# Kernel tuning notes

Measured on AMD Instinct MI355X. Metric: run time of the kernel, lower is better.

Reference implementation:

```python
import jax, jax.numpy as jnp
import numpy as np

NUM_PTS = 1024
LATENT_SIZE = 32
BETA = 0.1


def setup_inputs() -> dict:
    key = jax.random.key(0)
    k1, k2, k3, k4 = jax.random.split(key, 4)
    B = 128
    return {
        "recon_x": jax.random.normal(k1, (B, NUM_PTS, 3), dtype=jnp.float32),
        "x": jax.random.normal(k2, (B, NUM_PTS, 3), dtype=jnp.float32),
        "mu": jax.random.normal(k3, (B, LATENT_SIZE), dtype=jnp.float32),
        "logvar": jax.random.normal(k4, (B, LATENT_SIZE), dtype=jnp.float32),
    }


def _chamfer(recon_x, x):
    # Batched squared pairwise distances: P[b, i, j] = ||x[b,i] - recon_x[b,j]||^2
    xx = jnp.sum(x * x, axis=-1)              # [B, N]
    yy = jnp.sum(recon_x * recon_x, axis=-1)  # [B, N]
    xy = jnp.einsum("bnd,bmd->bnm", x, recon_x)  # [B, N, N]
    P = xx[:, :, None] + yy[:, None, :] - 2.0 * xy
    # Bidirectional min + sum
    loss_1 = jnp.sum(jnp.min(P, axis=1))  # for each recon point, nearest x point
    loss_2 = jnp.sum(jnp.min(P, axis=2))  # for each x point, nearest recon point
    return loss_1 + loss_2


def reference(recon_x, x, mu, logvar):
    RE = _chamfer(recon_x, x) / NUM_PTS
    KLD = -0.5 * jnp.sum(1.0 + logvar - mu * mu - jnp.exp(logvar))
    KLD = KLD / LATENT_SIZE
    return RE + KLD * BETA
```

## Files before the change

kernel.cpp:

```cpp
#include <hip/hip_runtime.h>

#define NUM_PTS 1024
#define NBATCH 128
#define BTHREADS 128
#define THREADS 256
#define NCHUNK 8
#define CHUNK_PTS (NUM_PTS / NCHUNK)
#define CHAMF_SCALE (1.0f / 1024.0f)
#define KLD_SCALE   (-0.5f * 0.1f / 32.0f)

#define WS_CHUNK_STRIDE (NBATCH * NUM_PTS)
#define WS_DIR_STRIDE   (NCHUNK * WS_CHUNK_STRIDE)

__global__ __launch_bounds__(BTHREADS, 4) void chamfer_part(
    const float* __restrict__ recon_x,
    const float* __restrict__ x,
    float* __restrict__ ws)
{
    const int b     = blockIdx.x >> 4;
    const int sub   = blockIdx.x & 15;
    const int dir   = sub >> 3;
    const int chunk = sub & 7;

    const float* rp = (dir == 0 ? x : recon_x) + (size_t)b * NUM_PTS * 3;
    const float* qp = (dir == 0 ? recon_x : x) + (size_t)b * NUM_PTS * 3
                      + chunk * CHUNK_PTS * 3;

    __shared__ float sq[4][CHUNK_PTS];
    {
        const int p = threadIdx.x;
        const float qx = qp[3 * p + 0];
        const float qy = qp[3 * p + 1];
        const float qz = qp[3 * p + 2];
        sq[0][p] = qx;
        sq[1][p] = qy;
        sq[2][p] = qz;
        sq[3][p] = fmaf(qx, qx, fmaf(qy, qy, qz * qz));
    }

    float buf[24];
    {
        const float4* __restrict__ src = (const float4*)(rp + 24 * threadIdx.x);
        float4* bp = (float4*)buf;
#pragma unroll
        for (int i = 0; i < 6; ++i) bp[i] = src[i];
    }
    float vx[8], vy[8], vz[8], r2[8], m[8];
#pragma unroll
    for (int k = 0; k < 8; ++k) {
        const float px = buf[3 * k + 0];
        const float py = buf[3 * k + 1];
        const float pz = buf[3 * k + 2];
        r2[k] = fmaf(px, px, fmaf(py, py, pz * pz));
        vx[k] = -2.0f * px;
        vy[k] = -2.0f * py;
        vz[k] = -2.0f * pz;
        m[k]  = 1e30f;
    }
    __syncthreads();

    const float4* __restrict__ sx4 = (const float4*)sq[0];
    const float4* __restrict__ sy4 = (const float4*)sq[1];
    const float4* __restrict__ sz4 = (const float4*)sq[2];
    const float4* __restrict__ s24 = (const float4*)sq[3];
#pragma unroll 2
    for (int t = 0; t < CHUNK_PTS / 4; ++t) {
        const float4 qx = sx4[t];
        const float4 qy = sy4[t];
        const float4 qz = sz4[t];
        const float4 q2 = s24[t];
#pragma unroll
        for (int jp = 0; jp < 2; ++jp) {
            const int j0 = 2 * jp, j1 = 2 * jp + 1;
            const float ax0 = (&qx.x)[j0], ay0 = (&qy.x)[j0],
                        az0 = (&qz.x)[j0], aq0 = (&q2.x)[j0];
            const float ax1 = (&qx.x)[j1], ay1 = (&qy.x)[j1],
                        az1 = (&qz.x)[j1], aq1 = (&q2.x)[j1];
            float d0[8], d1[8];
#pragma unroll
            for (int r = 0; r < 8; ++r)
                d0[r] = fmaf(vx[r], ax0, fmaf(vy[r], ay0, fmaf(vz[r], az0, aq0)));
#pragma unroll
            for (int r = 0; r < 8; ++r)
                d1[r] = fmaf(vx[r], ax1, fmaf(vy[r], ay1, fmaf(vz[r], az1, aq1)));
#pragma unroll
            for (int r = 0; r < 8; ++r)
                m[r] = fminf(fminf(m[r], d0[r]), d1[r]);
        }
    }

    float4* dst = (float4*)(ws + dir * WS_DIR_STRIDE + chunk * WS_CHUNK_STRIDE
                            + b * NUM_PTS + 8 * threadIdx.x);
    dst[0] = make_float4(r2[0] + m[0], r2[1] + m[1], r2[2] + m[2], r2[3] + m[3]);
    dst[1] = make_float4(r2[4] + m[4], r2[5] + m[5], r2[6] + m[6], r2[7] + m[7]);
}

__global__ __launch_bounds__(THREADS) void reduce_kernel(
    const float* __restrict__ ws,
    const float* __restrict__ mu,
    const float* __restrict__ logvar,
    float* __restrict__ out)
{
    const int gid  = blockIdx.x * THREADS + threadIdx.x;
    const int base = gid * 4;
    const int dir  = base >> 17;
    const int rem  = base & 131071;

    const float4* p = (const float4*)(ws + dir * WS_DIR_STRIDE + rem);
    float4 mn = p[0];
#pragma unroll
    for (int c = 1; c < NCHUNK; ++c) {
        const float4 q = p[c * (WS_CHUNK_STRIDE / 4)];
        mn.x = fminf(mn.x, q.x);
        mn.y = fminf(mn.y, q.y);
        mn.z = fminf(mn.z, q.z);
        mn.w = fminf(mn.w, q.w);
    }
    float v = (mn.x + mn.y + mn.z + mn.w) * CHAMF_SCALE;

    if (blockIdx.x < 16) {
        const int t = blockIdx.x * THREADS + threadIdx.x;
        const float lv = logvar[t];
        const float mm = mu[t];
        v += (1.0f + lv - mm * mm - expf(lv)) * KLD_SCALE;
    }

    for (int off = 32; off > 0; off >>= 1)
        v += __shfl_down(v, off, 64);

    __shared__ float red[THREADS / 64];
    const int lane = threadIdx.x & 63;
    const int wv   = threadIdx.x >> 6;
    if (lane == 0) red[wv] = v;
    __syncthreads();
    if (threadIdx.x == 0) {
        float sum = 0.f;
        for (int w = 0; w < THREADS / 64; ++w) sum += red[w];
        atomicAdd(out, sum);
    }
}

extern "C" void kernel_launch(void* const* d_in, const int* in_sizes, int n_in,
                              void* d_out, int out_size, void* d_ws, size_t ws_size,
                              hipStream_t stream) {
    const float* recon_x = (const float*)d_in[0];
    const float* x       = (const float*)d_in[1];
    const float* mu      = (const float*)d_in[2];
    const float* logvar  = (const float*)d_in[3];
    float* out = (float*)d_out;
    float* ws  = (float*)d_ws;

    hipMemsetAsync(out, 0, sizeof(float), stream);

    chamfer_part<<<NBATCH * 2 * NCHUNK, BTHREADS, 0, stream>>>(recon_x, x, ws);
    reduce_kernel<<<256, THREADS, 0, stream>>>(ws, mu, logvar, out);
}
```

Measured before the change: 91.94 us.

## Compute both Chamfer directions from one distance pass per tile

Each distance tile is now evaluated once and used for both directions: row minima are kept in registers, and column minima are built through shuffles and a shared-memory reduction. The separate reverse-direction pass goes away, which halves the pairwise distance arithmetic. A prep kernel packs recon_x into an xyz plus squared-norm layout that the main kernel reads through constant-address-space pointers (scalar loads) instead of staging it in LDS. The cost is an extra kernel launch, per-pair shuffles and LDS writes for the column minima, and one atomic per block.

```diff
diff --git a/kernel.cpp b/kernel.cpp
--- a/kernel.cpp
+++ b/kernel.cpp
@@ -1,116 +1,137 @@
 #include <hip/hip_runtime.h>
+#include <stdint.h>
 
 #define NUM_PTS 1024
 #define NBATCH 128
 #define BTHREADS 128
-#define THREADS 256
-#define NCHUNK 8
-#define CHUNK_PTS (NUM_PTS / NCHUNK)
+#define RTHREADS 256
+#define NJC 16
+#define JC_PTS 64
 #define CHAMF_SCALE (1.0f / 1024.0f)
 #define KLD_SCALE   (-0.5f * 0.1f / 32.0f)
 
-#define WS_CHUNK_STRIDE (NBATCH * NUM_PTS)
-#define WS_DIR_STRIDE   (NCHUNK * WS_CHUNK_STRIDE)
+#define QSOA_FLOATS   (NBATCH * NUM_PTS * 4)
+#define ROW_JC_STRIDE (NBATCH * NUM_PTS)
 
-__global__ __launch_bounds__(BTHREADS, 4) void chamfer_part(
-    const float* __restrict__ recon_x,
+typedef const __attribute__((address_space(4))) float* cfp;
+
+__global__ __launch_bounds__(RTHREADS) void prep_kernel(
+    const float* __restrict__ recon_x, float* __restrict__ qsoa)
+{
+    const int b = blockIdx.x;
+    const float4* __restrict__ src = (const float4*)(recon_x + (size_t)b * NUM_PTS * 3);
+    float4* __restrict__ dst = (float4*)qsoa + (size_t)b * NUM_PTS;
+    const int t = threadIdx.x;
+    const float4 A = src[3 * t + 0];
+    const float4 B = src[3 * t + 1];
+    const float4 C = src[3 * t + 2];
+    dst[4 * t + 0] = make_float4(A.x, A.y, A.z, fmaf(A.x, A.x, fmaf(A.y, A.y, A.z * A.z)));
+    dst[4 * t + 1] = make_float4(A.w, B.x, B.y, fmaf(A.w, A.w, fmaf(B.x, B.x, B.y * B.y)));
+    dst[4 * t + 2] = make_float4(B.z, B.w, C.x, fmaf(B.z, B.z, fmaf(B.w, B.w, C.x * C.x)));
+    dst[4 * t + 3] = make_float4(C.y, C.z, C.w, fmaf(C.y, C.y, fmaf(C.z, C.z, C.w * C.w)));
+}
+
+__global__ __launch_bounds__(BTHREADS, 4) void chamfer_sym(
     const float* __restrict__ x,
-    float* __restrict__ ws)
+    const float* __restrict__ qsoa,
+    float* __restrict__ ws_row,
+    float* __restrict__ out)
 {
-    const int b     = blockIdx.x >> 4;
-    const int sub   = blockIdx.x & 15;
-    const int dir   = sub >> 3;
-    const int chunk = sub & 7;
+    const int b  = blockIdx.x >> 4;
+    const int jc = blockIdx.x & 15;
+    const int tid = threadIdx.x;
+    const int slot = tid >> 1;
 
-    const float* rp = (dir == 0 ? x : recon_x) + (size_t)b * NUM_PTS * 3;
-    const float* qp = (dir == 0 ? recon_x : x) + (size_t)b * NUM_PTS * 3
-                      + chunk * CHUNK_PTS * 3;
+    cfp qs = (cfp)(uintptr_t)(qsoa + ((size_t)b * NUM_PTS + jc * JC_PTS) * 4);
 
-    __shared__ float sq[4][CHUNK_PTS];
-    {
-        const int p = threadIdx.x;
-        const float qx = qp[3 * p + 0];
-        const float qy = qp[3 * p + 1];
-        const float qz = qp[3 * p + 2];
-        sq[0][p] = qx;
-        sq[1][p] = qy;
-        sq[2][p] = qz;
-        sq[3][p] = fmaf(qx, qx, fmaf(qy, qy, qz * qz));
-    }
-
+    const float* rp = x + (size_t)b * NUM_PTS * 3;
     float buf[24];
     {
-        const float4* __restrict__ src = (const float4*)(rp + 24 * threadIdx.x);
+        const float4* __restrict__ s4 = (const float4*)(rp + 24 * tid);
         float4* bp = (float4*)buf;
 #pragma unroll
-        for (int i = 0; i < 6; ++i) bp[i] = src[i];
+        for (int i = 0; i < 6; ++i) bp[i] = s4[i];
     }
     float vx[8], vy[8], vz[8], r2[8], m[8];
 #pragma unroll
     for (int k = 0; k < 8; ++k) {
-        const float px = buf[3 * k + 0];
-        const float py = buf[3 * k + 1];
-        const float pz = buf[3 * k + 2];
+        const float px = buf[3 * k], py = buf[3 * k + 1], pz = buf[3 * k + 2];
         r2[k] = fmaf(px, px, fmaf(py, py, pz * pz));
         vx[k] = -2.0f * px;
         vy[k] = -2.0f * py;
         vz[k] = -2.0f * pz;
         m[k]  = 1e30f;
     }
-    __syncthreads();
 
-    const float4* __restrict__ sx4 = (const float4*)sq[0];
-    const float4* __restrict__ sy4 = (const float4*)sq[1];
-    const float4* __restrict__ sz4 = (const float4*)sq[2];
-    const float4* __restrict__ s24 = (const float4*)sq[3];
+    __shared__ float scol[JC_PTS][65];
+    __shared__ float red[2];
+
+    auto pair_eval = [&](float qax, float qay, float qaz, float qaw,
+                         float qbx, float qby, float qbz, float qbw,
+                         int ja, int jb) {
+        float d0[8], d1[8];
+#pragma unroll
+        for (int r = 0; r < 8; ++r)
+            d0[r] = fmaf(vx[r], qax, fmaf(vy[r], qay, fmaf(vz[r], qaz, r2[r])));
+#pragma unroll
+        for (int r = 0; r < 8; ++r)
+            d1[r] = fmaf(vx[r], qbx, fmaf(vy[r], qby, fmaf(vz[r], qbz, r2[r])));
+#pragma unroll
+        for (int r = 0; r < 8; ++r)
+            m[r] = fminf(fminf(m[r], d0[r] + qaw), d1[r] + qbw);
+        float c0 = fminf(fminf(fminf(d0[0], d0[1]), fminf(d0[2], d0[3])),
+                         fminf(fminf(d0[4], d0[5]), fminf(d0[6], d0[7]))) + qaw;
+        float c1 = fminf(fminf(fminf(d1[0], d1[1]), fminf(d1[2], d1[3])),
+                         fminf(fminf(d1[4], d1[5]), fminf(d1[6], d1[7]))) + qbw;
+        c0 = fminf(c0, __shfl_xor(c0, 1, 64));
+        c1 = fminf(c1, __shfl_xor(c1, 1, 64));
+        if (!(tid & 1)) { scol[ja][slot] = c0; scol[jb][slot] = c1; }
+    };
+
 #pragma unroll 2
-    for (int t = 0; t < CHUNK_PTS / 4; ++t) {
-        const float4 qx = sx4[t];
-        const float4 qy = sy4[t];
-        const float4 qz = sz4[t];
-        const float4 q2 = s24[t];
-#pragma unroll
-        for (int jp = 0; jp < 2; ++jp) {
-            const int j0 = 2 * jp, j1 = 2 * jp + 1;
-            const float ax0 = (&qx.x)[j0], ay0 = (&qy.x)[j0],
-                        az0 = (&qz.x)[j0], aq0 = (&q2.x)[j0];
-            const float ax1 = (&qx.x)[j1], ay1 = (&qy.x)[j1],
-                        az1 = (&qz.x)[j1], aq1 = (&q2.x)[j1];
-            float d0[8], d1[8];
-#pragma unroll
-            for (int r = 0; r < 8; ++r)
-                d0[r] = fmaf(vx[r], ax0, fmaf(vy[r], ay0, fmaf(vz[r], az0, aq0)));
-#pragma unroll
-            for (int r = 0; r < 8; ++r)
-                d1[r] = fmaf(vx[r], ax1, fmaf(vy[r], ay1, fmaf(vz[r], az1, aq1)));
-#pragma unroll
-            for (int r = 0; r < 8; ++r)
-                m[r] = fminf(fminf(m[r], d0[r]), d1[r]);
-        }
+    for (int g = 0; g < 16; ++g) {
+        const int o = 16 * g;
+        const float a0 = qs[o + 0],  a1 = qs[o + 1],  a2 = qs[o + 2],  a3 = qs[o + 3];
+        const float b0 = qs[o + 4],  b1 = qs[o + 5],  b2 = qs[o + 6],  b3 = qs[o + 7];
+        const float c0 = qs[o + 8],  c1 = qs[o + 9],  c2 = qs[o + 10], c3 = qs[o + 11];
+        const float e0 = qs[o + 12], e1 = qs[o + 13], e2 = qs[o + 14], e3 = qs[o + 15];
+        pair_eval(a0, a1, a2, a3, b0, b1, b2, b3, 4 * g + 0, 4 * g + 1);
+        pair_eval(c0, c1, c2, c3, e0, e1, e2, e3, 4 * g + 2, 4 * g + 3);
     }
 
-    float4* dst = (float4*)(ws + dir * WS_DIR_STRIDE + chunk * WS_CHUNK_STRIDE
-                            + b * NUM_PTS + 8 * threadIdx.x);
-    dst[0] = make_float4(r2[0] + m[0], r2[1] + m[1], r2[2] + m[2], r2[3] + m[3]);
-    dst[1] = make_float4(r2[4] + m[4], r2[5] + m[5], r2[6] + m[6], r2[7] + m[7]);
+    float4* dst = (float4*)(ws_row + (size_t)jc * ROW_JC_STRIDE + b * NUM_PTS + 8 * tid);
+    dst[0] = make_float4(m[0], m[1], m[2], m[3]);
+    dst[1] = make_float4(m[4], m[5], m[6], m[7]);
+
+    __syncthreads();
+    {
+        const int j = tid >> 1, h = tid & 1;
+        float cm = scol[j][h * 32];
+#pragma unroll
+        for (int k = 1; k < 32; ++k) cm = fminf(cm, scol[j][h * 32 + k]);
+        cm = fminf(cm, __shfl_xor(cm, 1, 64));
+        float v = (h == 0) ? cm * CHAMF_SCALE : 0.0f;
+        for (int off = 32; off > 0; off >>= 1)
+            v += __shfl_down(v, off, 64);
+        if ((tid & 63) == 0) red[tid >> 6] = v;
+        __syncthreads();
+        if (tid == 0) atomicAdd(out, red[0] + red[1]);
+    }
 }
 
-__global__ __launch_bounds__(THREADS) void reduce_kernel(
-    const float* __restrict__ ws,
+__global__ __launch_bounds__(RTHREADS) void reduce_kernel(
+    const float* __restrict__ ws_row,
     const float* __restrict__ mu,
     const float* __restrict__ logvar,
     float* __restrict__ out)
 {
-    const int gid  = blockIdx.x * THREADS + threadIdx.x;
-    const int base = gid * 4;
-    const int dir  = base >> 17;
-    const int rem  = base & 131071;
-
-    const float4* p = (const float4*)(ws + dir * WS_DIR_STRIDE + rem);
+    const int b  = blockIdx.x;
+    const int iv = threadIdx.x * 4;
+    const float4* p = (const float4*)(ws_row + (size_t)b * NUM_PTS + iv);
     float4 mn = p[0];
 #pragma unroll
-    for (int c = 1; c < NCHUNK; ++c) {
-        const float4 q = p[c * (WS_CHUNK_STRIDE / 4)];
+    for (int c = 1; c < NJC; ++c) {
+        const float4 q = p[c * (ROW_JC_STRIDE / 4)];
         mn.x = fminf(mn.x, q.x);
         mn.y = fminf(mn.y, q.y);
         mn.z = fminf(mn.z, q.z);
@@ -119,7 +140,7 @@
     float v = (mn.x + mn.y + mn.z + mn.w) * CHAMF_SCALE;
 
     if (blockIdx.x < 16) {
-        const int t = blockIdx.x * THREADS + threadIdx.x;
+        const int t = blockIdx.x * RTHREADS + threadIdx.x;
         const float lv = logvar[t];
         const float mm = mu[t];
         v += (1.0f + lv - mm * mm - expf(lv)) * KLD_SCALE;
@@ -128,14 +149,14 @@
     for (int off = 32; off > 0; off >>= 1)
         v += __shfl_down(v, off, 64);
 
-    __shared__ float red[THREADS / 64];
+    __shared__ float red[RTHREADS / 64];
     const int lane = threadIdx.x & 63;
     const int wv   = threadIdx.x >> 6;
     if (lane == 0) red[wv] = v;
     __syncthreads();
     if (threadIdx.x == 0) {
         float sum = 0.f;
-        for (int w = 0; w < THREADS / 64; ++w) sum += red[w];
+        for (int w = 0; w < RTHREADS / 64; ++w) sum += red[w];
         atomicAdd(out, sum);
     }
 }
@@ -147,11 +168,13 @@
     const float* x       = (const float*)d_in[1];
     const float* mu      = (const float*)d_in[2];
     const float* logvar  = (const float*)d_in[3];
-    float* out = (float*)d_out;
-    float* ws  = (float*)d_ws;
+    float* out    = (float*)d_out;
+    float* qsoa   = (float*)d_ws;
+    float* ws_row = (float*)d_ws + QSOA_FLOATS;
 
-    hipMemsetAsync(out, 0, sizeof(float), stream);
+    (void)hipMemsetAsync(out, 0, sizeof(float), stream);
 
-    chamfer_part<<<NBATCH * 2 * NCHUNK, BTHREADS, 0, stream>>>(recon_x, x, ws);
-    reduce_kernel<<<256, THREADS, 0, stream>>>(ws, mu, logvar, out);
+    prep_kernel<<<NBATCH, RTHREADS, 0, stream>>>(recon_x, qsoa);
+    chamfer_sym<<<NBATCH * NJC, BTHREADS, 0, stream>>>(x, qsoa, ws_row, out);
+    reduce_kernel<<<NBATCH, RTHREADS, 0, stream>>>(ws_row, mu, logvar, out);
 }
```

Result: slower. 108.9 us (+18.5%).

## Split chamfer directions across wavefronts with 16 rows per thread

Applied to the files above, without the earlier changes.

Each block now handles both directions for one batch and one 64-point query chunk, one wavefront per direction. Each thread keeps 16 reference points in registers instead of 8, so every shared-memory query load feeds twice as many FMAs. The number of query chunks doubles to 16, which doubles the workspace and the reduce kernel's min-over-chunks traffic. Register pressure rises with 16 accumulators per thread, which may limit occupancy.

```diff
diff --git a/kernel.cpp b/kernel.cpp
--- a/kernel.cpp
+++ b/kernel.cpp
@@ -2,115 +2,111 @@
 
 #define NUM_PTS 1024
 #define NBATCH 128
-#define BTHREADS 128
-#define THREADS 256
-#define NCHUNK 8
-#define CHUNK_PTS (NUM_PTS / NCHUNK)
+#define BT 128
+#define RT 256
+#define NJC 16
+#define JC 64
+#define R 16
 #define CHAMF_SCALE (1.0f / 1024.0f)
 #define KLD_SCALE   (-0.5f * 0.1f / 32.0f)
 
-#define WS_CHUNK_STRIDE (NBATCH * NUM_PTS)
-#define WS_DIR_STRIDE   (NCHUNK * WS_CHUNK_STRIDE)
+#define WS_CHUNK (NBATCH * NUM_PTS)
+#define WS_DIR   (NJC * WS_CHUNK)
 
-__global__ __launch_bounds__(BTHREADS, 4) void chamfer_part(
+__global__ __launch_bounds__(BT, 4) void chamfer_part(
     const float* __restrict__ recon_x,
     const float* __restrict__ x,
     float* __restrict__ ws)
 {
-    const int b     = blockIdx.x >> 4;
-    const int sub   = blockIdx.x & 15;
-    const int dir   = sub >> 3;
-    const int chunk = sub & 7;
+    const int b  = blockIdx.x >> 4;
+    const int c  = blockIdx.x & 15;
+    const int w  = threadIdx.x >> 6;
+    const int lt = threadIdx.x & 63;
 
-    const float* rp = (dir == 0 ? x : recon_x) + (size_t)b * NUM_PTS * 3;
-    const float* qp = (dir == 0 ? recon_x : x) + (size_t)b * NUM_PTS * 3
-                      + chunk * CHUNK_PTS * 3;
-
-    __shared__ float sq[4][CHUNK_PTS];
+    __shared__ float sq[2][4][JC];
     {
-        const int p = threadIdx.x;
-        const float qx = qp[3 * p + 0];
-        const float qy = qp[3 * p + 1];
-        const float qz = qp[3 * p + 2];
-        sq[0][p] = qx;
-        sq[1][p] = qy;
-        sq[2][p] = qz;
-        sq[3][p] = fmaf(qx, qx, fmaf(qy, qy, qz * qz));
+        const float* qsrc = (w == 0 ? recon_x : x)
+                            + (size_t)b * NUM_PTS * 3 + (size_t)c * JC * 3 + 3 * lt;
+        const float qx = qsrc[0], qy = qsrc[1], qz = qsrc[2];
+        sq[w][0][lt] = qx;
+        sq[w][1][lt] = qy;
+        sq[w][2][lt] = qz;
+        sq[w][3][lt] = fmaf(qx, qx, fmaf(qy, qy, qz * qz));
     }
 
-    float buf[24];
+    const float* rp = (w == 0 ? x : recon_x) + (size_t)b * NUM_PTS * 3;
+    float vx[R], vy[R], vz[R], m[R];
     {
-        const float4* __restrict__ src = (const float4*)(rp + 24 * threadIdx.x);
+        const float4* __restrict__ s4 = (const float4*)(rp + 48 * lt);
+        float buf[48];
         float4* bp = (float4*)buf;
 #pragma unroll
-        for (int i = 0; i < 6; ++i) bp[i] = src[i];
-    }
-    float vx[8], vy[8], vz[8], r2[8], m[8];
+        for (int i = 0; i < 12; ++i) bp[i] = s4[i];
 #pragma unroll
-    for (int k = 0; k < 8; ++k) {
-        const float px = buf[3 * k + 0];
-        const float py = buf[3 * k + 1];
-        const float pz = buf[3 * k + 2];
-        r2[k] = fmaf(px, px, fmaf(py, py, pz * pz));
-        vx[k] = -2.0f * px;
-        vy[k] = -2.0f * py;
-        vz[k] = -2.0f * pz;
-        m[k]  = 1e30f;
+        for (int k = 0; k < R; ++k) {
+            vx[k] = -2.0f * buf[3 * k + 0];
+            vy[k] = -2.0f * buf[3 * k + 1];
+            vz[k] = -2.0f * buf[3 * k + 2];
+            m[k]  = 1e30f;
+        }
     }
     __syncthreads();
 
-    const float4* __restrict__ sx4 = (const float4*)sq[0];
-    const float4* __restrict__ sy4 = (const float4*)sq[1];
-    const float4* __restrict__ sz4 = (const float4*)sq[2];
-    const float4* __restrict__ s24 = (const float4*)sq[3];
+    const float4* __restrict__ qxp = (const float4*)sq[w][0];
+    const float4* __restrict__ qyp = (const float4*)sq[w][1];
+    const float4* __restrict__ qzp = (const float4*)sq[w][2];
+    const float4* __restrict__ q2p = (const float4*)sq[w][3];
 #pragma unroll 2
-    for (int t = 0; t < CHUNK_PTS / 4; ++t) {
-        const float4 qx = sx4[t];
-        const float4 qy = sy4[t];
-        const float4 qz = sz4[t];
-        const float4 q2 = s24[t];
+    for (int g = 0; g < JC / 4; ++g) {
+        const float4 qx = qxp[g];
+        const float4 qy = qyp[g];
+        const float4 qz = qzp[g];
+        const float4 q2 = q2p[g];
 #pragma unroll
-        for (int jp = 0; jp < 2; ++jp) {
-            const int j0 = 2 * jp, j1 = 2 * jp + 1;
-            const float ax0 = (&qx.x)[j0], ay0 = (&qy.x)[j0],
-                        az0 = (&qz.x)[j0], aq0 = (&q2.x)[j0];
-            const float ax1 = (&qx.x)[j1], ay1 = (&qy.x)[j1],
-                        az1 = (&qz.x)[j1], aq1 = (&q2.x)[j1];
-            float d0[8], d1[8];
+        for (int r = 0; r < R; ++r) {
+            const float d0 = fmaf(vx[r], qx.x, fmaf(vy[r], qy.x, fmaf(vz[r], qz.x, q2.x)));
+            const float d1 = fmaf(vx[r], qx.y, fmaf(vy[r], qy.y, fmaf(vz[r], qz.y, q2.y)));
+            m[r] = fminf(fminf(m[r], d0), d1);
+        }
 #pragma unroll
-            for (int r = 0; r < 8; ++r)
-                d0[r] = fmaf(vx[r], ax0, fmaf(vy[r], ay0, fmaf(vz[r], az0, aq0)));
-#pragma unroll
-            for (int r = 0; r < 8; ++r)
-                d1[r] = fmaf(vx[r], ax1, fmaf(vy[r], ay1, fmaf(vz[r], az1, aq1)));
-#pragma unroll
-            for (int r = 0; r < 8; ++r)
-                m[r] = fminf(fminf(m[r], d0[r]), d1[r]);
+        for (int r = 0; r < R; ++r) {
+            const float d2 = fmaf(vx[r], qx.z, fmaf(vy[r], qy.z, fmaf(vz[r], qz.z, q2.z)));
+            const float d3 = fmaf(vx[r], qx.w, fmaf(vy[r], qy.w, fmaf(vz[r], qz.w, q2.w)));
+            m[r] = fminf(fminf(m[r], d2), d3);
         }
     }
 
-    float4* dst = (float4*)(ws + dir * WS_DIR_STRIDE + chunk * WS_CHUNK_STRIDE
-                            + b * NUM_PTS + 8 * threadIdx.x);
-    dst[0] = make_float4(r2[0] + m[0], r2[1] + m[1], r2[2] + m[2], r2[3] + m[3]);
-    dst[1] = make_float4(r2[4] + m[4], r2[5] + m[5], r2[6] + m[6], r2[7] + m[7]);
+    float4* dst = (float4*)(ws + (size_t)w * WS_DIR + (size_t)c * WS_CHUNK
+                            + b * NUM_PTS + 16 * lt);
+#pragma unroll
+    for (int k4 = 0; k4 < 4; ++k4) {
+        float o[4];
+#pragma unroll
+        for (int i = 0; i < 4; ++i) {
+            const int k = 4 * k4 + i;
+            const float r2 = 0.25f * fmaf(vx[k], vx[k], fmaf(vy[k], vy[k], vz[k] * vz[k]));
+            o[i] = r2 + m[k];
+        }
+        dst[k4] = make_float4(o[0], o[1], o[2], o[3]);
+    }
 }
 
-__global__ __launch_bounds__(THREADS) void reduce_kernel(
+__global__ __launch_bounds__(RT) void reduce_kernel(
     const float* __restrict__ ws,
     const float* __restrict__ mu,
     const float* __restrict__ logvar,
     float* __restrict__ out)
 {
-    const int gid  = blockIdx.x * THREADS + threadIdx.x;
+    const int gid  = blockIdx.x * RT + threadIdx.x;
     const int base = gid * 4;
     const int dir  = base >> 17;
     const int rem  = base & 131071;
 
-    const float4* p = (const float4*)(ws + dir * WS_DIR_STRIDE + rem);
+    const float4* p = (const float4*)(ws + (size_t)dir * WS_DIR + rem);
     float4 mn = p[0];
 #pragma unroll
-    for (int c = 1; c < NCHUNK; ++c) {
-        const float4 q = p[c * (WS_CHUNK_STRIDE / 4)];
+    for (int c = 1; c < NJC; ++c) {
+        const float4 q = p[c * (WS_CHUNK / 4)];
         mn.x = fminf(mn.x, q.x);
         mn.y = fminf(mn.y, q.y);
         mn.z = fminf(mn.z, q.z);
@@ -119,7 +115,7 @@
     float v = (mn.x + mn.y + mn.z + mn.w) * CHAMF_SCALE;
 
     if (blockIdx.x < 16) {
-        const int t = blockIdx.x * THREADS + threadIdx.x;
+        const int t = blockIdx.x * RT + threadIdx.x;
         const float lv = logvar[t];
         const float mm = mu[t];
         v += (1.0f + lv - mm * mm - expf(lv)) * KLD_SCALE;
@@ -128,14 +124,14 @@
     for (int off = 32; off > 0; off >>= 1)
         v += __shfl_down(v, off, 64);
 
-    __shared__ float red[THREADS / 64];
+    __shared__ float red[RT / 64];
     const int lane = threadIdx.x & 63;
     const int wv   = threadIdx.x >> 6;
     if (lane == 0) red[wv] = v;
     __syncthreads();
     if (threadIdx.x == 0) {
         float sum = 0.f;
-        for (int w = 0; w < THREADS / 64; ++w) sum += red[w];
+        for (int wq = 0; wq < RT / 64; ++wq) sum += red[wq];
         atomicAdd(out, sum);
     }
 }
@@ -150,8 +146,8 @@
     float* out = (float*)d_out;
     float* ws  = (float*)d_ws;
 
-    hipMemsetAsync(out, 0, sizeof(float), stream);
+    (void)hipMemsetAsync(out, 0, sizeof(float), stream);
 
-    chamfer_part<<<NBATCH * 2 * NCHUNK, BTHREADS, 0, stream>>>(recon_x, x, ws);
-    reduce_kernel<<<256, THREADS, 0, stream>>>(ws, mu, logvar, out);
+    chamfer_part<<<NBATCH * NJC, BT, 0, stream>>>(recon_x, x, ws);
+    reduce_kernel<<<256, RT, 0, stream>>>(ws, mu, logvar, out);
 }
```

After: 93.86 us. 2.1% more time.
